# Performance work log

Hardware: AMD Instinct MI355X
Metric: run time of the kernel (lower is better)

Reference implementation:

```python
import jax, jax.numpy as jnp
import numpy as np

N, L, D = 8192, 50, 64          # batch nodes, history length, embed_dim
NUM_ITEMS, NUM_ATTRS, NUM_FAM = 50000, 100000, 100000


def setup_inputs() -> dict:
    key = jax.random.key(0)
    ks = jax.random.split(key, 12)
    scale = 0.05
    return {
        "nodes": jax.random.randint(ks[0], (N,), 0, NUM_ITEMS),
        "history_va": jax.random.randint(ks[1], (N, L), 0, NUM_ATTRS),
        "history_af": jax.random.randint(ks[2], (N, L), 0, NUM_FAM),
        "v2e_w": jax.random.normal(ks[3], (NUM_ITEMS, D), jnp.float32) * scale,
        "a2e_w": jax.random.normal(ks[4], (NUM_ATTRS, D), jnp.float32) * scale,
        "f2e_w": jax.random.normal(ks[5], (NUM_FAM, D), jnp.float32) * scale,
        "W1": jax.random.normal(ks[6], (3 * D, D), jnp.float32) * scale,
        "b1": jnp.zeros((D,), jnp.float32),
        "W2": jax.random.normal(ks[7], (D, D), jnp.float32) * scale,
        "b2": jnp.zeros((D,), jnp.float32),
        "w3": jax.random.normal(ks[8], (D, 1), jnp.float32) * scale,
        "b3": jnp.zeros((1,), jnp.float32),
    }


def reference(nodes, history_va, history_af, v2e_w, a2e_w, f2e_w,
              W1, b1, W2, b2, w3, b3):
    # Batched form of the per-node loop (va=True branch).
    e_va = a2e_w[history_va]                       # [N, L, D] gathered attr embeds
    e_af = f2e_w[history_af]                       # [N, L, D] gathered famous embeds
    va_rep = v2e_w[nodes]                          # [N, D]    target item embed
    rep = jnp.broadcast_to(va_rep[:, None, :], e_va.shape)
    x = jnp.concatenate([e_va, rep, e_af], axis=-1)  # [N, L, 3D]
    h = jax.nn.relu(x @ W1 + b1)                   # [N, L, D]
    h = jax.nn.relu(h @ W2 + b2)                   # [N, L, D]
    scores = (h @ w3 + b3)[..., 0]                 # [N, L]
    att = jax.nn.softmax(scores, axis=1)           # softmax over history dim
    # e_va.T @ att per node  ==  weighted sum over history
    return jnp.einsum("nld,nl->nd", e_va, att)     # [N, D]
```

## Files before the change

kernel.cpp:

```cpp
#include <hip/hip_runtime.h>
#include <hip/hip_bf16.h>

typedef __bf16 bf16x8 __attribute__((ext_vector_type(8)));
typedef __bf16 bf16x4 __attribute__((ext_vector_type(4)));
typedef float  f32x4  __attribute__((ext_vector_type(4)));

#define HL 50
#define DD 64


__global__ __launch_bounds__(256, 4) void prep_embed_kernel(
    const float* __restrict__ src, const float* __restrict__ W1part,
    __bf16* __restrict__ dst, int nrows)
{
    __shared__ __align__(16) __bf16 es[64 * 72];
    const int tid = threadIdx.x;
    const int w = tid >> 6, lane = tid & 63, lq = lane & 15, quad = lane >> 4;
    const int col = w * 16 + lq;
    const int r0 = blockIdx.x * 64;

    #pragma unroll
    for (int i = 0; i < 4; ++i) {
        int t = i * 256 + tid;
        int row = t >> 4, q = t & 15;
        int gr = r0 + row; if (gr >= nrows) gr = nrows - 1;
        float4 v = *(const float4*)(src + (size_t)gr * DD + q * 4);
        bf16x4 pk = {(__bf16)v.x, (__bf16)v.y, (__bf16)v.z, (__bf16)v.w};
        *(bf16x4*)&es[row * 72 + q * 4] = pk;
    }
    bf16x8 bfr[2];
    #pragma unroll
    for (int t = 0; t < 2; ++t)
        #pragma unroll
        for (int j = 0; j < 8; ++j)
            bfr[t][j] = (__bf16)W1part[(t * 32 + quad * 8 + j) * DD + col];
    __syncthreads();

    f32x4 acc[4];
    #pragma unroll
    for (int mt = 0; mt < 4; ++mt) acc[mt] = (f32x4){0.f, 0.f, 0.f, 0.f};
    #pragma unroll
    for (int t = 0; t < 2; ++t)
        #pragma unroll
        for (int mt = 0; mt < 4; ++mt) {
            bf16x8 a = *(const bf16x8*)&es[(mt * 16 + lq) * 72 + t * 32 + quad * 8];
            acc[mt] = __builtin_amdgcn_mfma_f32_16x16x32_bf16(a, bfr[t], acc[mt], 0, 0, 0);
        }
    __syncthreads();
    #pragma unroll
    for (int mt = 0; mt < 4; ++mt)
        #pragma unroll
        for (int r = 0; r < 4; ++r)
            es[(mt * 16 + quad * 4 + r) * 72 + col] = (__bf16)acc[mt][r];
    __syncthreads();
    {
        int row = tid >> 2, seg = tid & 3;
        int gr = r0 + row;
        if (gr < nrows) {
            bf16x8 vv = *(const bf16x8*)&es[row * 72 + seg * 16];
            *(bf16x8*)(dst + (size_t)gr * DD + seg * 16) = vv;
        }
    }
}

__global__ __launch_bounds__(256, 4) void prep_bias_kernel(
    const int* __restrict__ nodes, const float* __restrict__ v2e,
    const float* __restrict__ W1, const float* __restrict__ b1,
    float* __restrict__ ba, int N)
{
    __shared__ __align__(16) __bf16 rs[64 * 72];
    const int tid = threadIdx.x;
    const int w = tid >> 6, lane = tid & 63, lq = lane & 15, quad = lane >> 4;
    const int col = w * 16 + lq;
    const int n0 = blockIdx.x * 64;

    #pragma unroll
    for (int i = 0; i < 4; ++i) {
        int t = i * 256 + tid;
        int row = t >> 4, q = t & 15;
        int gn = n0 + row; if (gn >= N) gn = N - 1;
        int idx = nodes[gn];
        float4 v = *(const float4*)(v2e + (size_t)idx * DD + q * 4);
        bf16x4 pk = {(__bf16)v.x, (__bf16)v.y, (__bf16)v.z, (__bf16)v.w};
        *(bf16x4*)&rs[row * 72 + q * 4] = pk;
    }
    bf16x8 bfr[2];
    #pragma unroll
    for (int t = 0; t < 2; ++t)
        #pragma unroll
        for (int j = 0; j < 8; ++j)
            bfr[t][j] = (__bf16)W1[(64 + t * 32 + quad * 8 + j) * DD + col];
    const float b1c = b1[col];
    __syncthreads();

    f32x4 acc[4];
    #pragma unroll
    for (int mt = 0; mt < 4; ++mt) acc[mt] = (f32x4){0.f, 0.f, 0.f, 0.f};
    #pragma unroll
    for (int t = 0; t < 2; ++t)
        #pragma unroll
        for (int mt = 0; mt < 4; ++mt) {
            bf16x8 a = *(const bf16x8*)&rs[(mt * 16 + lq) * 72 + t * 32 + quad * 8];
            acc[mt] = __builtin_amdgcn_mfma_f32_16x16x32_bf16(a, bfr[t], acc[mt], 0, 0, 0);
        }
    #pragma unroll
    for (int mt = 0; mt < 4; ++mt)
        #pragma unroll
        for (int r = 0; r < 4; ++r) {
            int gn = n0 + mt * 16 + quad * 4 + r;
            if (gn < N) ba[(size_t)gn * DD + col] = acc[mt][r] + b1c;
        }
}

__global__ __launch_bounds__(256) void prep_frag_kernel(
    const float* __restrict__ W2, const float* __restrict__ w3,
    const float* __restrict__ b2,
    __bf16* __restrict__ w2f, float* __restrict__ wsc)
{
    const int tid = threadIdx.x;
    const int ln = tid & 63, c0 = tid >> 6;
    #pragma unroll
    for (int h = 0; h < 2; ++h) {
        int combo = c0 + 4 * h;
        int ct = combo >> 1, t = combo & 1;
        __bf16* d = w2f + ((size_t)combo * 64 + ln) * 8;
        #pragma unroll
        for (int j = 0; j < 8; ++j)
            d[j] = (__bf16)W2[(t * 32 + (ln >> 4) * 8 + j) * DD + ct * 16 + (ln & 15)];
    }
    if (tid < 64) { wsc[tid] = w3[tid]; wsc[64 + tid] = b2[tid]; }
}

__global__ __launch_bounds__(256, 8) void va_main_kernel(
    const int*    __restrict__ hva,
    const int*    __restrict__ haf,
    const __bf16* __restrict__ A2,
    const __bf16* __restrict__ F2,
    const float*  __restrict__ eva,
    const float*  __restrict__ ba,
    const __bf16* __restrict__ w2f,
    const float*  __restrict__ wsc,
    float*        __restrict__ out)
{
    __shared__ float pbuf[64];
    __shared__ float ps[4 * 64];

    const int tid  = threadIdx.x;
    const int w    = tid >> 6;
    const int lane = tid & 63;
    const int lq   = lane & 15;
    const int quad = lane >> 4;
    const int node = blockIdx.x;
    const int* hb = hva + node * HL;
    const int* fb = haf + node * HL;

    const int lr = min(w * 16 + lq, HL - 1);
    const int ia = hb[lr];
    const int ifm = fb[lr];
    bf16x8 a2g[2], f2g[2];
    f32x4  bb[4];
    #pragma unroll
    for (int t = 0; t < 2; ++t) {
        a2g[t] = *(const bf16x8*)(A2 + (size_t)ia  * DD + t * 32 + quad * 8);
        f2g[t] = *(const bf16x8*)(F2 + (size_t)ifm * DD + t * 32 + quad * 8);
        bb[t * 2]     = *(const f32x4*)(ba + (size_t)node * DD + t * 32 + quad * 8);
        bb[t * 2 + 1] = *(const f32x4*)(ba + (size_t)node * DD + t * 32 + quad * 8 + 4);
    }

    bf16x8 h1f[2];
    #pragma unroll
    for (int t = 0; t < 2; ++t)
        #pragma unroll
        for (int j = 0; j < 8; ++j) {
            float f = (float)a2g[t][j] + (float)f2g[t][j] + bb[t * 2 + (j >> 2)][j & 3];
            h1f[t][j] = (__bf16)fmaxf(f, 0.f);
        }

    float srow[4] = {0.f, 0.f, 0.f, 0.f};
    #pragma unroll
    for (int ct = 0; ct < 4; ++ct) {
        const float b2c = wsc[64 + ct * 16 + lq];
        f32x4 acc = {b2c, b2c, b2c, b2c};
        #pragma unroll
        for (int t = 0; t < 2; ++t) {
            bf16x8 bfr = *(const bf16x8*)(w2f + ((size_t)(ct * 2 + t) * 64 + lane) * 8);
            acc = __builtin_amdgcn_mfma_f32_16x16x32_bf16(h1f[t], bfr, acc, 0, 0, 0);
        }
        const float w3c = wsc[ct * 16 + lq];
        #pragma unroll
        for (int r = 0; r < 4; ++r)
            srow[r] = fmaf(fmaxf(acc[r], 0.f), w3c, srow[r]);
    }
    #pragma unroll
    for (int r = 0; r < 4; ++r) {
        #pragma unroll
        for (int m = 1; m < 16; m <<= 1) srow[r] += __shfl_xor(srow[r], m);
    }
    if (lq == 0) {
        #pragma unroll
        for (int r = 0; r < 4; ++r) pbuf[w * 16 + quad * 4 + r] = srow[r];
    }

    int   oidx[13];
    float ev[13];
    #pragma unroll
    for (int i = 0; i < 13; ++i) {
        int l = w + 4 * i;
        oidx[i] = hb[(l < HL) ? l : 0];
    }
    #pragma unroll
    for (int i = 0; i < 13; ++i)
        ev[i] = eva[(size_t)oidx[i] * DD + lane];
    __syncthreads();

    float att;
    {
        float s = (lane < HL) ? pbuf[lane] : -3.0e38f;
        float mx = s;
        #pragma unroll
        for (int m = 1; m < 64; m <<= 1) mx = fmaxf(mx, __shfl_xor(mx, m));
        float e = (lane < HL) ? __expf(s - mx) : 0.f;
        float sm = e;
        #pragma unroll
        for (int m = 1; m < 64; m <<= 1) sm += __shfl_xor(sm, m);
        att = e / sm;
    }

    float o = 0.f;
    #pragma unroll
    for (int i = 0; i < 13; ++i) {
        int l = w + 4 * i;
        if (l < HL) {
            float av = __shfl(att, l);
            o = fmaf(av, ev[i], o);
        }
    }
    ps[w * 64 + lane] = o;
    __syncthreads();
    if (w == 0)
        out[(size_t)node * DD + lane] =
            ps[lane] + ps[64 + lane] + ps[128 + lane] + ps[192 + lane];
}

#define FMR  112
#define FMT  7
#define FXSS 136

__global__ __launch_bounds__(256) void fb_prep_kernel(
    const float* __restrict__ W1, const float* __restrict__ W2,
    const float* __restrict__ w3, const float* __restrict__ b1,
    const float* __restrict__ b2,
    __bf16* __restrict__ wf, float* __restrict__ wsc)
{
    const int tid  = threadIdx.x;
    const int quad = tid >> 6;
    const int col  = tid & 63;
    __bf16* dst = wf + tid * 64;
    #pragma unroll
    for (int t = 0; t < 4; ++t)
        #pragma unroll
        for (int j = 0; j < 8; ++j) {
            int keff = t * 32 + quad * 8 + j;
            int krow = (keff < 64) ? keff : keff + 64;
            dst[t * 8 + j] = (__bf16)W1[krow * 64 + col];
        }
    #pragma unroll
    for (int t = 0; t < 2; ++t)
        #pragma unroll
        for (int j = 0; j < 8; ++j) {
            dst[32 + t * 8 + j] = (__bf16)W1[(64 + t * 32 + quad * 8 + j) * 64 + col];
            dst[48 + t * 8 + j] = (__bf16)W2[(t * 32 + quad * 8 + j) * 64 + col];
        }
    if (tid < 64) {
        wsc[tid] = w3[tid]; wsc[64 + tid] = b1[tid]; wsc[128 + tid] = b2[tid];
    }
}

__global__ __launch_bounds__(256, 5) void fb_agg_kernel(
    const int* __restrict__ nodes, const int* __restrict__ hva,
    const int* __restrict__ haf, const float* __restrict__ v2e,
    const float* __restrict__ a2e, const float* __restrict__ f2e,
    const __bf16* __restrict__ wf, const float* __restrict__ wsc,
    float* __restrict__ out)
{
    __shared__ __bf16 xs[FMR * FXSS];
    __shared__ float  pbuf[4 * FMR];
    const int tid = threadIdx.x;
    const int w = tid >> 6, lane = tid & 63, lq = lane & 15, quad = lane >> 4;
    const int col = w * 16 + lq;
    const int n0 = blockIdx.x * 2;
    {
        const int* hb = hva + n0 * HL;
        const int* fb = haf + n0 * HL;
        #pragma unroll
        for (int i = 0; i < 13; ++i) {
            int t = i * 256 + tid;
            if (t < 2 * HL * 2 * 16) {
                int r = t >> 4, q = t & 15;
                bool va = (r < 2 * HL);
                int gr = va ? r : r - 2 * HL;
                int idx = va ? hb[gr] : fb[gr];
                const float* src = (va ? a2e : f2e) + (size_t)idx * DD + q * 4;
                float4 v = *(const float4*)src;
                bf16x4 pk = {(__bf16)v.x, (__bf16)v.y, (__bf16)v.z, (__bf16)v.w};
                *(bf16x4*)&xs[gr * FXSS + (va ? 0 : DD) + q * 4] = pk;
            }
        }
    }
    bf16x8 repf[2];
    #pragma unroll
    for (int t = 0; t < 2; ++t)
        #pragma unroll
        for (int j = 0; j < 8; ++j) repf[t][j] = (__bf16)0.f;
    if (lq < 2) {
        int nd = nodes[n0 + lq];
        const float* rp = v2e + (size_t)nd * DD;
        #pragma unroll
        for (int t = 0; t < 2; ++t) {
            float4 v0 = *(const float4*)(rp + t * 32 + quad * 8);
            float4 v1 = *(const float4*)(rp + t * 32 + quad * 8 + 4);
            repf[t] = (bf16x8){(__bf16)v0.x, (__bf16)v0.y, (__bf16)v0.z, (__bf16)v0.w,
                               (__bf16)v1.x, (__bf16)v1.y, (__bf16)v1.z, (__bf16)v1.w};
        }
    }
    const __bf16* fbp = wf + (size_t)(quad * 64 + col) * 64;
    bf16x8 b1f[4], b1u[2], b2f[2];
    #pragma unroll
    for (int t = 0; t < 4; ++t) b1f[t] = *(const bf16x8*)(fbp + t * 8);
    #pragma unroll
    for (int t = 0; t < 2; ++t) {
        b1u[t] = *(const bf16x8*)(fbp + 32 + t * 8);
        b2f[t] = *(const bf16x8*)(fbp + 48 + t * 8);
    }
    const float w3c = wsc[col];
    const float b1c = wsc[64 + col];
    const float b2c = wsc[128 + col];
    f32x4 rb = {0.f, 0.f, 0.f, 0.f};
    #pragma unroll
    for (int t = 0; t < 2; ++t)
        rb = __builtin_amdgcn_mfma_f32_16x16x32_bf16(repf[t], b1u[t], rb, 0, 0, 0);
    const float bias0 = __shfl(rb[0], lq) + b1c;
    const float bias1 = __shfl(rb[1], lq) + b1c;
    __syncthreads();
    f32x4 acc[FMT];
    #pragma unroll
    for (int mt = 0; mt < FMT; ++mt)
        #pragma unroll
        for (int r = 0; r < 4; ++r) {
            int gr = mt * 16 + quad * 4 + r;
            acc[mt][r] = (gr >= HL) ? bias1 : bias0;
        }
    #pragma unroll
    for (int t = 0; t < 4; ++t)
        #pragma unroll
        for (int mt = 0; mt < FMT; ++mt) {
            bf16x8 a = *(const bf16x8*)&xs[(mt * 16 + lq) * FXSS + t * 32 + quad * 8];
            acc[mt] = __builtin_amdgcn_mfma_f32_16x16x32_bf16(a, b1f[t], acc[mt], 0, 0, 0);
        }
    __syncthreads();
    #pragma unroll
    for (int mt = 0; mt < FMT; ++mt)
        #pragma unroll
        for (int r = 0; r < 4; ++r) {
            int gr = mt * 16 + quad * 4 + r;
            xs[gr * FXSS + DD + col] = (__bf16)fmaxf(acc[mt][r], 0.f);
        }
    __syncthreads();
    f32x4 a2[FMT];
    #pragma unroll
    for (int mt = 0; mt < FMT; ++mt) a2[mt] = (f32x4){b2c, b2c, b2c, b2c};
    #pragma unroll
    for (int t = 0; t < 2; ++t)
        #pragma unroll
        for (int mt = 0; mt < FMT; ++mt) {
            bf16x8 a = *(const bf16x8*)&xs[(mt * 16 + lq) * FXSS + DD + t * 32 + quad * 8];
            a2[mt] = __builtin_amdgcn_mfma_f32_16x16x32_bf16(a, b2f[t], a2[mt], 0, 0, 0);
        }
    #pragma unroll
    for (int mt = 0; mt < FMT; ++mt) {
        float p0 = fmaxf(a2[mt][0], 0.f) * w3c;
        float p1 = fmaxf(a2[mt][1], 0.f) * w3c;
        float p2 = fmaxf(a2[mt][2], 0.f) * w3c;
        float p3 = fmaxf(a2[mt][3], 0.f) * w3c;
        #pragma unroll
        for (int m = 1; m < 16; m <<= 1) {
            p0 += __shfl_xor(p0, m); p1 += __shfl_xor(p1, m);
            p2 += __shfl_xor(p2, m); p3 += __shfl_xor(p3, m);
        }
        if (lq == 0) {
            int rowb = mt * 16 + quad * 4;
            pbuf[w * FMR + rowb + 0] = p0; pbuf[w * FMR + rowb + 1] = p1;
            pbuf[w * FMR + rowb + 2] = p2; pbuf[w * FMR + rowb + 3] = p3;
        }
    }
    __syncthreads();
    const int n = w & 1, lh = w >> 1;
    float att;
    {
        float s = -3.0e38f;
        if (lane < HL) {
            int gr = n * HL + lane;
            s = pbuf[gr] + pbuf[FMR + gr] + pbuf[2 * FMR + gr] + pbuf[3 * FMR + gr];
        }
        float mx = s;
        #pragma unroll
        for (int m = 1; m < 64; m <<= 1) mx = fmaxf(mx, __shfl_xor(mx, m));
        float e = (lane < HL) ? __expf(s - mx) : 0.f;
        float sm = e;
        #pragma unroll
        for (int m = 1; m < 64; m <<= 1) sm += __shfl_xor(sm, m);
        att = e / sm;
    }
    {
        float o = 0.f;
        const int lb = lh * 25;
        #pragma unroll
        for (int i = 0; i < 25; ++i) {
            int l = lb + i;
            float av = __shfl(att, l);
            o = fmaf(av, (float)xs[(n * HL + l) * FXSS + lane], o);
        }
        float* op = (float*)&xs[(100 + w) * FXSS + DD];
        op[lane] = o;
    }
    __syncthreads();
    if (w < 2) {
        const float* p0 = (const float*)&xs[(100 + w) * FXSS + DD];
        const float* p1 = (const float*)&xs[(100 + w + 2) * FXSS + DD];
        out[(size_t)(n0 + w) * DD + lane] = p0[lane] + p1[lane];
    }
}

extern "C" void kernel_launch(void* const* d_in, const int* in_sizes, int n_in,
                              void* d_out, int out_size, void* d_ws, size_t ws_size,
                              hipStream_t stream) {
    const int*   nodes = (const int*)d_in[0];
    const int*   hva   = (const int*)d_in[1];
    const int*   haf   = (const int*)d_in[2];
    const float* v2e   = (const float*)d_in[3];
    const float* a2e   = (const float*)d_in[4];
    const float* f2e   = (const float*)d_in[5];
    const float* W1    = (const float*)d_in[6];
    const float* b1    = (const float*)d_in[7];
    const float* W2    = (const float*)d_in[8];
    const float* b2    = (const float*)d_in[9];
    const float* w3    = (const float*)d_in[10];
    float* out = (float*)d_out;

    const int N  = in_sizes[0];
    const int nA = in_sizes[4] / DD;
    const int nF = in_sizes[5] / DD;

    size_t offA2 = 0;
    size_t offF2 = (offA2 + (size_t)nA * DD * 2 + 255) & ~(size_t)255;
    size_t offBA = (offF2 + (size_t)nF * DD * 2 + 255) & ~(size_t)255;
    size_t offWF = (offBA + (size_t)N * DD * 4 + 255) & ~(size_t)255;
    size_t offSC = offWF + 8 * 64 * 8 * 2;
    size_t need  = offSC + 128 * 4;

    if (ws_size >= need) {
        __bf16* A2  = (__bf16*)((char*)d_ws + offA2);
        __bf16* F2  = (__bf16*)((char*)d_ws + offF2);
        float*  ba  = (float*)((char*)d_ws + offBA);
        __bf16* w2f = (__bf16*)((char*)d_ws + offWF);
        float*  wsc = (float*)((char*)d_ws + offSC);

        prep_frag_kernel<<<1, 256, 0, stream>>>(W2, w3, b2, w2f, wsc);
        prep_bias_kernel<<<(N + 63) / 64, 256, 0, stream>>>(nodes, v2e, W1, b1, ba, N);
        prep_embed_kernel<<<(nA + 63) / 64, 256, 0, stream>>>(a2e, W1, A2, nA);
        prep_embed_kernel<<<(nF + 63) / 64, 256, 0, stream>>>(f2e, W1 + 128 * DD, F2, nF);
        va_main_kernel<<<N, 256, 0, stream>>>(hva, haf, A2, F2, a2e, ba, w2f, wsc, out);
    } else {
        __bf16* wf  = (__bf16*)d_ws;
        float*  wsc = (float*)((char*)d_ws + 256 * 64 * 2);
        fb_prep_kernel<<<1, 256, 0, stream>>>(W1, W2, w3, b1, b2, wf, wsc);
        fb_agg_kernel<<<N / 2, 256, 0, stream>>>(nodes, hva, haf, v2e, a2e, f2e,
                                                 wf, wsc, out);
    }
}
```

Measured before the change: 164.7 us.

## Fuse prep kernels into one launch and switch intermediates to fp16

Merges the three prep kernels (four launches) into a single prep_all kernel that dispatches on block index. All precomputed tables move from bf16/fp32 to fp16, the bias table shrinks to fp16, and an extra fp16 copy of the attribute embeddings is written so the final weighted sum gathers half-width rows instead of fp32 ones. The main kernel adds the fp16 vectors directly, skips gathers for padded history rows, and broadcasts history indices with shuffles instead of reloading them. This cuts launch overhead and gather bandwidth, but adds a write of another 100000x64 fp16 table in prep and lowers precision of the output path.

```diff
diff --git a/kernel.cpp b/kernel.cpp
--- a/kernel.cpp
+++ b/kernel.cpp
@@ -1,146 +1,153 @@
 #include <hip/hip_runtime.h>
 #include <hip/hip_bf16.h>
 
-typedef __bf16 bf16x8 __attribute__((ext_vector_type(8)));
-typedef __bf16 bf16x4 __attribute__((ext_vector_type(4)));
-typedef float  f32x4  __attribute__((ext_vector_type(4)));
+typedef __bf16    bf16x8 __attribute__((ext_vector_type(8)));
+typedef __bf16    bf16x4 __attribute__((ext_vector_type(4)));
+typedef _Float16  f16x8  __attribute__((ext_vector_type(8)));
+typedef _Float16  f16x4  __attribute__((ext_vector_type(4)));
+typedef float     f32x4  __attribute__((ext_vector_type(4)));
 
 #define HL 50
 #define DD 64
 
 
-__global__ __launch_bounds__(256, 4) void prep_embed_kernel(
-    const float* __restrict__ src, const float* __restrict__ W1part,
-    __bf16* __restrict__ dst, int nrows)
+__global__ __launch_bounds__(256, 4) void prep_all_kernel(
+    const int*   __restrict__ nodes,
+    const float* __restrict__ v2e,
+    const float* __restrict__ a2e,
+    const float* __restrict__ f2e,
+    const float* __restrict__ W1,
+    const float* __restrict__ b1,
+    const float* __restrict__ W2,
+    const float* __restrict__ b2,
+    const float* __restrict__ w3,
+    _Float16* __restrict__ A2, _Float16* __restrict__ F2,
+    _Float16* __restrict__ E16, _Float16* __restrict__ ba16,
+    _Float16* __restrict__ w2f, float* __restrict__ wsc,
+    int nA, int nF, int N, int GA, int GF, int GB)
 {
-    __shared__ __align__(16) __bf16 es[64 * 72];
-    const int tid = threadIdx.x;
-    const int w = tid >> 6, lane = tid & 63, lq = lane & 15, quad = lane >> 4;
-    const int col = w * 16 + lq;
-    const int r0 = blockIdx.x * 64;
-
-    #pragma unroll
-    for (int i = 0; i < 4; ++i) {
-        int t = i * 256 + tid;
-        int row = t >> 4, q = t & 15;
-        int gr = r0 + row; if (gr >= nrows) gr = nrows - 1;
-        float4 v = *(const float4*)(src + (size_t)gr * DD + q * 4);
-        bf16x4 pk = {(__bf16)v.x, (__bf16)v.y, (__bf16)v.z, (__bf16)v.w};
-        *(bf16x4*)&es[row * 72 + q * 4] = pk;
-    }
-    bf16x8 bfr[2];
-    #pragma unroll
-    for (int t = 0; t < 2; ++t)
-        #pragma unroll
-        for (int j = 0; j < 8; ++j)
-            bfr[t][j] = (__bf16)W1part[(t * 32 + quad * 8 + j) * DD + col];
-    __syncthreads();
-
-    f32x4 acc[4];
-    #pragma unroll
-    for (int mt = 0; mt < 4; ++mt) acc[mt] = (f32x4){0.f, 0.f, 0.f, 0.f};
-    #pragma unroll
-    for (int t = 0; t < 2; ++t)
-        #pragma unroll
-        for (int mt = 0; mt < 4; ++mt) {
-            bf16x8 a = *(const bf16x8*)&es[(mt * 16 + lq) * 72 + t * 32 + quad * 8];
-            acc[mt] = __builtin_amdgcn_mfma_f32_16x16x32_bf16(a, bfr[t], acc[mt], 0, 0, 0);
-        }
-    __syncthreads();
-    #pragma unroll
-    for (int mt = 0; mt < 4; ++mt)
-        #pragma unroll
-        for (int r = 0; r < 4; ++r)
-            es[(mt * 16 + quad * 4 + r) * 72 + col] = (__bf16)acc[mt][r];
-    __syncthreads();
-    {
-        int row = tid >> 2, seg = tid & 3;
-        int gr = r0 + row;
-        if (gr < nrows) {
-            bf16x8 vv = *(const bf16x8*)&es[row * 72 + seg * 16];
-            *(bf16x8*)(dst + (size_t)gr * DD + seg * 16) = vv;
-        }
+    __shared__ __align__(16) _Float16 es[64 * 72];
+    const int tid  = threadIdx.x;
+    const int w    = tid >> 6, lane = tid & 63;
+    const int lq   = lane & 15, quad = lane >> 4;
+    const int col  = w * 16 + lq;
+    const int bid  = blockIdx.x;
+
+    if (bid < GA + GF) {
+        const bool  isA   = (bid < GA);
+        const int   rb    = isA ? bid : bid - GA;
+        const int   nrows = isA ? nA : nF;
+        const float* src  = isA ? a2e : f2e;
+        const float* Wp   = isA ? W1 : (W1 + 128 * DD);
+        _Float16*   dst   = isA ? A2 : F2;
+        const int   r0    = rb * 64;
+
+        #pragma unroll
+        for (int i = 0; i < 4; ++i) {
+            int t = i * 256 + tid;
+            int row = t >> 4, q = t & 15;
+            int gr = r0 + row; if (gr >= nrows) gr = nrows - 1;
+            float4 v = *(const float4*)(src + (size_t)gr * DD + q * 4);
+            f16x4 pk = {(_Float16)v.x, (_Float16)v.y, (_Float16)v.z, (_Float16)v.w};
+            *(f16x4*)&es[row * 72 + q * 4] = pk;
+            if (isA) *(f16x4*)(E16 + (size_t)gr * DD + q * 4) = pk;
+        }
+        f16x8 bfr[2];
+        #pragma unroll
+        for (int t = 0; t < 2; ++t)
+            #pragma unroll
+            for (int j = 0; j < 8; ++j)
+                bfr[t][j] = (_Float16)Wp[(t * 32 + quad * 8 + j) * DD + col];
+        __syncthreads();
+
+        f32x4 acc[4];
+        #pragma unroll
+        for (int mt = 0; mt < 4; ++mt) acc[mt] = (f32x4){0.f, 0.f, 0.f, 0.f};
+        #pragma unroll
+        for (int t = 0; t < 2; ++t)
+            #pragma unroll
+            for (int mt = 0; mt < 4; ++mt) {
+                f16x8 a = *(const f16x8*)&es[(mt * 16 + lq) * 72 + t * 32 + quad * 8];
+                acc[mt] = __builtin_amdgcn_mfma_f32_16x16x32_f16(a, bfr[t], acc[mt], 0, 0, 0);
+            }
+        __syncthreads();
+        #pragma unroll
+        for (int mt = 0; mt < 4; ++mt)
+            #pragma unroll
+            for (int r = 0; r < 4; ++r)
+                es[(mt * 16 + quad * 4 + r) * 72 + col] = (_Float16)acc[mt][r];
+        __syncthreads();
+        {
+            int row = tid >> 2, seg = tid & 3;
+            int gr = r0 + row;
+            if (gr < nrows) {
+                f16x8 vv = *(const f16x8*)&es[row * 72 + seg * 16];
+                *(f16x8*)(dst + (size_t)gr * DD + seg * 16) = vv;
+            }
+        }
+    } else if (bid < GA + GF + GB) {
+        const int n0 = (bid - GA - GF) * 64;
+        #pragma unroll
+        for (int i = 0; i < 4; ++i) {
+            int t = i * 256 + tid;
+            int row = t >> 4, q = t & 15;
+            int gn = n0 + row; if (gn >= N) gn = N - 1;
+            int idx = nodes[gn];
+            float4 v = *(const float4*)(v2e + (size_t)idx * DD + q * 4);
+            f16x4 pk = {(_Float16)v.x, (_Float16)v.y, (_Float16)v.z, (_Float16)v.w};
+            *(f16x4*)&es[row * 72 + q * 4] = pk;
+        }
+        f16x8 bfr[2];
+        #pragma unroll
+        for (int t = 0; t < 2; ++t)
+            #pragma unroll
+            for (int j = 0; j < 8; ++j)
+                bfr[t][j] = (_Float16)W1[(64 + t * 32 + quad * 8 + j) * DD + col];
+        const float b1c = b1[col];
+        __syncthreads();
+
+        f32x4 acc[4];
+        #pragma unroll
+        for (int mt = 0; mt < 4; ++mt) acc[mt] = (f32x4){0.f, 0.f, 0.f, 0.f};
+        #pragma unroll
+        for (int t = 0; t < 2; ++t)
+            #pragma unroll
+            for (int mt = 0; mt < 4; ++mt) {
+                f16x8 a = *(const f16x8*)&es[(mt * 16 + lq) * 72 + t * 32 + quad * 8];
+                acc[mt] = __builtin_amdgcn_mfma_f32_16x16x32_f16(a, bfr[t], acc[mt], 0, 0, 0);
+            }
+        #pragma unroll
+        for (int mt = 0; mt < 4; ++mt)
+            #pragma unroll
+            for (int r = 0; r < 4; ++r) {
+                int gn = n0 + mt * 16 + quad * 4 + r;
+                if (gn < N) ba16[(size_t)gn * DD + col] = (_Float16)(acc[mt][r] + b1c);
+            }
+    } else {
+        const int ln = tid & 63, c0 = tid >> 6;
+        #pragma unroll
+        for (int h = 0; h < 2; ++h) {
+            int combo = c0 + 4 * h;
+            int ct = combo >> 1, t = combo & 1;
+            _Float16* d = w2f + ((size_t)combo * 64 + ln) * 8;
+            #pragma unroll
+            for (int j = 0; j < 8; ++j)
+                d[j] = (_Float16)W2[(t * 32 + (ln >> 4) * 8 + j) * DD + ct * 16 + (ln & 15)];
+        }
+        if (tid < 64) { wsc[tid] = w3[tid]; wsc[64 + tid] = b2[tid]; }
     }
 }
 
-__global__ __launch_bounds__(256, 4) void prep_bias_kernel(
-    const int* __restrict__ nodes, const float* __restrict__ v2e,
-    const float* __restrict__ W1, const float* __restrict__ b1,
-    float* __restrict__ ba, int N)
-{
-    __shared__ __align__(16) __bf16 rs[64 * 72];
-    const int tid = threadIdx.x;
-    const int w = tid >> 6, lane = tid & 63, lq = lane & 15, quad = lane >> 4;
-    const int col = w * 16 + lq;
-    const int n0 = blockIdx.x * 64;
-
-    #pragma unroll
-    for (int i = 0; i < 4; ++i) {
-        int t = i * 256 + tid;
-        int row = t >> 4, q = t & 15;
-        int gn = n0 + row; if (gn >= N) gn = N - 1;
-        int idx = nodes[gn];
-        float4 v = *(const float4*)(v2e + (size_t)idx * DD + q * 4);
-        bf16x4 pk = {(__bf16)v.x, (__bf16)v.y, (__bf16)v.z, (__bf16)v.w};
-        *(bf16x4*)&rs[row * 72 + q * 4] = pk;
-    }
-    bf16x8 bfr[2];
-    #pragma unroll
-    for (int t = 0; t < 2; ++t)
-        #pragma unroll
-        for (int j = 0; j < 8; ++j)
-            bfr[t][j] = (__bf16)W1[(64 + t * 32 + quad * 8 + j) * DD + col];
-    const float b1c = b1[col];
-    __syncthreads();
-
-    f32x4 acc[4];
-    #pragma unroll
-    for (int mt = 0; mt < 4; ++mt) acc[mt] = (f32x4){0.f, 0.f, 0.f, 0.f};
-    #pragma unroll
-    for (int t = 0; t < 2; ++t)
-        #pragma unroll
-        for (int mt = 0; mt < 4; ++mt) {
-            bf16x8 a = *(const bf16x8*)&rs[(mt * 16 + lq) * 72 + t * 32 + quad * 8];
-            acc[mt] = __builtin_amdgcn_mfma_f32_16x16x32_bf16(a, bfr[t], acc[mt], 0, 0, 0);
-        }
-    #pragma unroll
-    for (int mt = 0; mt < 4; ++mt)
-        #pragma unroll
-        for (int r = 0; r < 4; ++r) {
-            int gn = n0 + mt * 16 + quad * 4 + r;
-            if (gn < N) ba[(size_t)gn * DD + col] = acc[mt][r] + b1c;
-        }
-}
-
-__global__ __launch_bounds__(256) void prep_frag_kernel(
-    const float* __restrict__ W2, const float* __restrict__ w3,
-    const float* __restrict__ b2,
-    __bf16* __restrict__ w2f, float* __restrict__ wsc)
-{
-    const int tid = threadIdx.x;
-    const int ln = tid & 63, c0 = tid >> 6;
-    #pragma unroll
-    for (int h = 0; h < 2; ++h) {
-        int combo = c0 + 4 * h;
-        int ct = combo >> 1, t = combo & 1;
-        __bf16* d = w2f + ((size_t)combo * 64 + ln) * 8;
-        #pragma unroll
-        for (int j = 0; j < 8; ++j)
-            d[j] = (__bf16)W2[(t * 32 + (ln >> 4) * 8 + j) * DD + ct * 16 + (ln & 15)];
-    }
-    if (tid < 64) { wsc[tid] = w3[tid]; wsc[64 + tid] = b2[tid]; }
-}
-
 __global__ __launch_bounds__(256, 8) void va_main_kernel(
-    const int*    __restrict__ hva,
-    const int*    __restrict__ haf,
-    const __bf16* __restrict__ A2,
-    const __bf16* __restrict__ F2,
-    const float*  __restrict__ eva,
-    const float*  __restrict__ ba,
-    const __bf16* __restrict__ w2f,
-    const float*  __restrict__ wsc,
-    float*        __restrict__ out)
+    const int*      __restrict__ hva,
+    const int*      __restrict__ haf,
+    const _Float16* __restrict__ A2,
+    const _Float16* __restrict__ F2,
+    const _Float16* __restrict__ E16,
+    const _Float16* __restrict__ ba16,
+    const _Float16* __restrict__ w2f,
+    const float*    __restrict__ wsc,
+    float*          __restrict__ out)
 {
     __shared__ float pbuf[64];
     __shared__ float ps[4 * 64];
@@ -154,27 +161,31 @@
     const int* hb = hva + node * HL;
     const int* fb = haf + node * HL;
 
-    const int lr = min(w * 16 + lq, HL - 1);
-    const int ia = hb[lr];
-    const int ifm = fb[lr];
-    bf16x8 a2g[2], f2g[2];
-    f32x4  bb[4];
-    #pragma unroll
-    for (int t = 0; t < 2; ++t) {
-        a2g[t] = *(const bf16x8*)(A2 + (size_t)ia  * DD + t * 32 + quad * 8);
-        f2g[t] = *(const bf16x8*)(F2 + (size_t)ifm * DD + t * 32 + quad * 8);
-        bb[t * 2]     = *(const f32x4*)(ba + (size_t)node * DD + t * 32 + quad * 8);
-        bb[t * 2 + 1] = *(const f32x4*)(ba + (size_t)node * DD + t * 32 + quad * 8 + 4);
-    }
-
-    bf16x8 h1f[2];
+    const int  lr0   = w * 16 + lq;
+    const bool valid = (lr0 < HL);
+    f16x8 h1f[2];
     #pragma unroll
     for (int t = 0; t < 2; ++t)
         #pragma unroll
-        for (int j = 0; j < 8; ++j) {
-            float f = (float)a2g[t][j] + (float)f2g[t][j] + bb[t * 2 + (j >> 2)][j & 3];
-            h1f[t][j] = (__bf16)fmaxf(f, 0.f);
-        }
+        for (int j = 0; j < 8; ++j) h1f[t][j] = (_Float16)0.f;
+    if (valid) {
+        const int ia  = hb[lr0];
+        const int ifm = fb[lr0];
+        f16x8 a2g[2], f2g[2], bag[2];
+        #pragma unroll
+        for (int t = 0; t < 2; ++t) {
+            a2g[t] = *(const f16x8*)(A2   + (size_t)ia   * DD + t * 32 + quad * 8);
+            f2g[t] = *(const f16x8*)(F2   + (size_t)ifm  * DD + t * 32 + quad * 8);
+            bag[t] = *(const f16x8*)(ba16 + (size_t)node * DD + t * 32 + quad * 8);
+        }
+        #pragma unroll
+        for (int t = 0; t < 2; ++t) {
+            f16x8 h = a2g[t] + f2g[t] + bag[t];
+            #pragma unroll
+            for (int j = 0; j < 8; ++j)
+                h1f[t][j] = (h[j] > (_Float16)0.f) ? h[j] : (_Float16)0.f;
+        }
+    }
 
     float srow[4] = {0.f, 0.f, 0.f, 0.f};
     #pragma unroll
@@ -183,8 +194,8 @@
         f32x4 acc = {b2c, b2c, b2c, b2c};
         #pragma unroll
         for (int t = 0; t < 2; ++t) {
-            bf16x8 bfr = *(const bf16x8*)(w2f + ((size_t)(ct * 2 + t) * 64 + lane) * 8);
-            acc = __builtin_amdgcn_mfma_f32_16x16x32_bf16(h1f[t], bfr, acc, 0, 0, 0);
+            f16x8 bfr = *(const f16x8*)(w2f + ((size_t)(ct * 2 + t) * 64 + lane) * 8);
+            acc = __builtin_amdgcn_mfma_f32_16x16x32_f16(h1f[t], bfr, acc, 0, 0, 0);
         }
         const float w3c = wsc[ct * 16 + lq];
         #pragma unroll
@@ -201,16 +212,16 @@
         for (int r = 0; r < 4; ++r) pbuf[w * 16 + quad * 4 + r] = srow[r];
     }
 
-    int   oidx[13];
+    const int iv = hb[(lane < HL) ? lane : 0];
     float ev[13];
     #pragma unroll
     for (int i = 0; i < 13; ++i) {
         int l = w + 4 * i;
-        oidx[i] = hb[(l < HL) ? l : 0];
-    }
-    #pragma unroll
-    for (int i = 0; i < 13; ++i)
-        ev[i] = eva[(size_t)oidx[i] * DD + lane];
+        if (l < HL) {
+            int idx = __shfl(iv, l);
+            ev[i] = (float)E16[(size_t)idx * DD + lane];
+        }
+    }
     __syncthreads();
 
     float att;
@@ -453,23 +464,27 @@
 
     size_t offA2 = 0;
     size_t offF2 = (offA2 + (size_t)nA * DD * 2 + 255) & ~(size_t)255;
-    size_t offBA = (offF2 + (size_t)nF * DD * 2 + 255) & ~(size_t)255;
-    size_t offWF = (offBA + (size_t)N * DD * 4 + 255) & ~(size_t)255;
+    size_t offE  = (offF2 + (size_t)nF * DD * 2 + 255) & ~(size_t)255;
+    size_t offBA = (offE  + (size_t)nA * DD * 2 + 255) & ~(size_t)255;
+    size_t offWF = (offBA + (size_t)N * DD * 2 + 255) & ~(size_t)255;
     size_t offSC = offWF + 8 * 64 * 8 * 2;
     size_t need  = offSC + 128 * 4;
 
     if (ws_size >= need) {
-        __bf16* A2  = (__bf16*)((char*)d_ws + offA2);
-        __bf16* F2  = (__bf16*)((char*)d_ws + offF2);
-        float*  ba  = (float*)((char*)d_ws + offBA);
-        __bf16* w2f = (__bf16*)((char*)d_ws + offWF);
-        float*  wsc = (float*)((char*)d_ws + offSC);
-
-        prep_frag_kernel<<<1, 256, 0, stream>>>(W2, w3, b2, w2f, wsc);
-        prep_bias_kernel<<<(N + 63) / 64, 256, 0, stream>>>(nodes, v2e, W1, b1, ba, N);
-        prep_embed_kernel<<<(nA + 63) / 64, 256, 0, stream>>>(a2e, W1, A2, nA);
-        prep_embed_kernel<<<(nF + 63) / 64, 256, 0, stream>>>(f2e, W1 + 128 * DD, F2, nF);
-        va_main_kernel<<<N, 256, 0, stream>>>(hva, haf, A2, F2, a2e, ba, w2f, wsc, out);
+        _Float16* A2  = (_Float16*)((char*)d_ws + offA2);
+        _Float16* F2  = (_Float16*)((char*)d_ws + offF2);
+        _Float16* E16 = (_Float16*)((char*)d_ws + offE);
+        _Float16* ba  = (_Float16*)((char*)d_ws + offBA);
+        _Float16* w2f = (_Float16*)((char*)d_ws + offWF);
+        float*    wsc = (float*)((char*)d_ws + offSC);
+
+        const int GA = (nA + 63) / 64;
+        const int GF = (nF + 63) / 64;
+        const int GB = (N + 63) / 64;
+        prep_all_kernel<<<GA + GF + GB + 1, 256, 0, stream>>>(
+            nodes, v2e, a2e, f2e, W1, b1, W2, b2, w3,
+            A2, F2, E16, ba, w2f, wsc, nA, nF, N, GA, GF, GB);
+        va_main_kernel<<<N, 256, 0, stream>>>(hva, haf, A2, F2, E16, ba, w2f, wsc, out);
     } else {
         __bf16* wf  = (__bf16*)d_ws;
         float*  wsc = (float*)((char*)d_ws + 256 * 64 * 2);
```

Result: faster. 160.0 us (-2.8%).
